# Kernel optimization log

Hardware: AMD Instinct MI355X
Metric: run time of the kernel (lower is better)

## Reference

```python
import jax, jax.numpy as jnp
import numpy as np


def setup_inputs() -> dict:
    key = jax.random.key(0)
    k1, k2 = jax.random.split(key)
    B, N, E, D = 8, 2048, 64, 128
    spatial_embedding = jax.random.normal(k1, (B, N, E), dtype=jnp.float32)
    z = jax.random.normal(k2, (B, N, D), dtype=jnp.float32)
    return {"spatial_embedding": spatial_embedding, "z": z}


def reference(spatial_embedding, z):
    # Pairwise squared L2 distance via ||a||^2 + ||b||^2 - 2 a.b
    # (same math as (e0-e1).norm(2,-1)**2, avoids [B,N,N,E] intermediate)
    sq = jnp.sum(spatial_embedding * spatial_embedding, axis=-1)  # [B,N]
    inner = jnp.einsum('bie,bje->bij', spatial_embedding, spatial_embedding)
    d2 = jnp.maximum(sq[:, :, None] + sq[:, None, :] - 2.0 * inner, 0.0)  # [B,N,N]
    sim = jnp.exp(-d2)
    attn = sim / jnp.sum(sim, axis=-1, keepdims=True)
    out = jnp.einsum('bij,bjd->bid', attn, z)
    return out
```

## Files before the change

### kernel.cpp

```cpp
#include <hip/hip_runtime.h>
#include <hip/hip_bf16.h>

#define BB 8
#define NN 2048
#define EE 64
#define DD 128
#define BN (BB * NN)

typedef __attribute__((ext_vector_type(8))) short short8v;
typedef __attribute__((ext_vector_type(4))) float float4v;

__device__ __forceinline__ short f2bf(float f) {
    __hip_bfloat16 h = __float2bfloat16(f);
    return *reinterpret_cast<short*>(&h);
}
__device__ __forceinline__ uint32_t pack2bf(float a, float b) {
    return (uint32_t)(uint16_t)f2bf(a) | ((uint32_t)(uint16_t)f2bf(b) << 16);
}

__global__ __launch_bounds__(256) void prep_kernel(const float* __restrict__ emb,
                                                   const float* __restrict__ z,
                                                   short* __restrict__ embq,
                                                   short* __restrict__ zq,
                                                   float* __restrict__ sq) {
    __shared__ float zl[64 * 129];
    const int bid = blockIdx.x;
    const int t = threadIdx.x;

    if (bid < 512) {
        int gid = bid * 256 + t;
        int s = gid & 63;
        int ke = (gid >> 6) & 1;
        int r16 = (gid >> 7) & 127;
        int b = gid >> 14;
        int i = r16 * 16 + (s & 15);
        int e0 = ke * 32 + ((s >> 4) & 3) * 8;
        const float4* src = reinterpret_cast<const float4*>(emb + ((size_t)(b * NN + i)) * EE + e0);
        float4 v0 = src[0], v1 = src[1];
        short8v o;
        o[0] = f2bf(v0.x); o[1] = f2bf(v0.y); o[2] = f2bf(v0.z); o[3] = f2bf(v0.w);
        o[4] = f2bf(v1.x); o[5] = f2bf(v1.y); o[6] = f2bf(v1.z); o[7] = f2bf(v1.w);
        *reinterpret_cast<short8v*>(embq + (size_t)gid * 8) = o;
    } else if (bid < 768) {
        int v = bid - 512;
        int b = v >> 5;
        int jt = v & 31;
        int jb = jt * 64;
#pragma unroll
        for (int k = 0; k < 8; ++k) {
            int idx = t + k * 256;
            int jl = idx >> 5, c4 = idx & 31;
            float4 w = reinterpret_cast<const float4*>(z + ((size_t)(b * NN + jb + jl)) * DD)[c4];
            float* p = &zl[jl * 129 + c4 * 4];
            p[0] = w.x; p[1] = w.y; p[2] = w.z; p[3] = w.w;
        }
        __syncthreads();
#pragma unroll
        for (int k = 0; k < 4; ++k) {
            int sid = t + k * 256;
            int blk = sid >> 6, s = sid & 63;
            int ktl = blk >> 3, nt = blk & 7;
            int d = nt * 16 + (s & 15);
            int jl = ktl * 32 + ((s >> 4) & 3) * 8;
            short8v o;
#pragma unroll
            for (int e = 0; e < 8; ++e) o[e] = f2bf(zl[(jl + e) * 129 + d]);
            *reinterpret_cast<short8v*>(zq + ((size_t)((b * 64 + jt * 2 + ktl) * 8 + nt) * 64 + s) * 8) = o;
        }
    } else {
        int v = bid - 768;
        int q = t & 15;
#pragma unroll
        for (int p = 0; p < 4; ++p) {
            int row = v * 64 + p * 16 + (t >> 4);
            float4 rv = reinterpret_cast<const float4*>(emb + (size_t)row * EE)[q];
            float a0 = __bfloat162float(__float2bfloat16(rv.x));
            float a1 = __bfloat162float(__float2bfloat16(rv.y));
            float a2 = __bfloat162float(__float2bfloat16(rv.z));
            float a3 = __bfloat162float(__float2bfloat16(rv.w));
            float s2 = a0 * a0 + a1 * a1 + a2 * a2 + a3 * a3;
#pragma unroll
            for (int off = 1; off < 16; off <<= 1) s2 += __shfl_xor(s2, off);
            if (q == 0) sq[row] = s2;
        }
    }
}

__global__ __launch_bounds__(256, 2) void attn_mfma(const short* __restrict__ embq,
                                                    const short* __restrict__ zq,
                                                    const float* __restrict__ sq,
                                                    float* __restrict__ outnum,
                                                    float* __restrict__ den,
                                                    int njs) {
    __shared__ short sU[4][2048];

    const int t = threadIdx.x;
    const int bid = blockIdx.x;
    const int b = bid & 7;
    const int q = bid >> 3;
    const int it = q & 15;
    const int js = q >> 4;
    const int ib = it * 128;
    const int w = t >> 6;
    const int l = t & 63;
    const int g = (l >> 4) & 3;
    const int c = l & 15;

    const short8v* embq8 = (const short8v*)embq;
    const short8v* zq8 = (const short8v*)zq;
    const float* sqB = sq + b * NN;

    const int ntiles = 32 / njs;
    const int jt0 = js * ntiles;
    const int jtEnd = jt0 + ntiles;

    short8v qkB[2][2];
#pragma unroll
    for (int m = 0; m < 2; ++m)
#pragma unroll
        for (int ke = 0; ke < 2; ++ke)
            qkB[m][ke] = embq8[((size_t)(b * 128 + it * 8 + w * 2 + m) * 2 + ke) * 64 + l];
    float sqi[2];
#pragma unroll
    for (int m = 0; m < 2; ++m) sqi[m] = sqB[ib + w * 32 + m * 16 + c];

    float dsum[2] = {0.f, 0.f};
    float4v acc[2][8];
#pragma unroll
    for (int m = 0; m < 2; ++m)
#pragma unroll
        for (int nt = 0; nt < 8; ++nt) acc[m][nt] = (float4v){0.f, 0.f, 0.f, 0.f};

    char* ptw = (char*)&sU[w][0];
    const int swz = (c & 7) << 4;

    for (int jt = jt0; jt < jtEnd; ++jt) {
        short8v a[4][2];
        float4 sqj[4];
#pragma unroll
        for (int J = 0; J < 4; ++J) {
            a[J][0] = embq8[((size_t)(b * 128 + jt * 4 + J) * 2 + 0) * 64 + l];
            a[J][1] = embq8[((size_t)(b * 128 + jt * 4 + J) * 2 + 1) * 64 + l];
            sqj[J] = *reinterpret_cast<const float4*>(sqB + jt * 64 + J * 16 + 4 * g);
        }

        bool anyLive = false;
#pragma unroll
        for (int J = 0; J < 4; ++J) {
            float d2[2][4];
            float mn = 1e30f;
#pragma unroll
            for (int m = 0; m < 2; ++m) {
                float4v sfr = (float4v){0.f, 0.f, 0.f, 0.f};
                sfr = __builtin_amdgcn_mfma_f32_16x16x32_bf16(a[J][0], qkB[m][0], sfr, 0, 0, 0);
                sfr = __builtin_amdgcn_mfma_f32_16x16x32_bf16(a[J][1], qkB[m][1], sfr, 0, 0, 0);
                d2[m][0] = fmaxf(fmaf(-2.0f, sfr[0], sqi[m] + sqj[J].x), 0.0f);
                d2[m][1] = fmaxf(fmaf(-2.0f, sfr[1], sqi[m] + sqj[J].y), 0.0f);
                d2[m][2] = fmaxf(fmaf(-2.0f, sfr[2], sqi[m] + sqj[J].z), 0.0f);
                d2[m][3] = fmaxf(fmaf(-2.0f, sfr[3], sqi[m] + sqj[J].w), 0.0f);
                mn = fminf(mn, fminf(fminf(d2[m][0], d2[m][1]), fminf(d2[m][2], d2[m][3])));
            }
            const bool live = !__all(mn > 13.8f);
#pragma unroll
            for (int m = 0; m < 2; ++m) {
                unsigned long long pword = 0ull;
                if (live) {
                    float p0 = __expf(-d2[m][0]);
                    float p1 = __expf(-d2[m][1]);
                    float p2 = __expf(-d2[m][2]);
                    float p3 = __expf(-d2[m][3]);
                    dsum[m] += (p0 + p1) + (p2 + p3);
                    pword = (unsigned long long)pack2bf(p0, p1) |
                            ((unsigned long long)pack2bf(p2, p3) << 32);
                }
                *reinterpret_cast<unsigned long long*>(
                    ptw + ((m * 2048 + c * 128 + g * 8) ^ swz ^ (J * 32))) = pword;
            }
            anyLive |= live;
        }

        if (anyLive) {
            short8v pa[2][2];
#pragma unroll
            for (int m = 0; m < 2; ++m)
#pragma unroll
                for (int kt = 0; kt < 2; ++kt)
                    pa[m][kt] = *reinterpret_cast<const short8v*>(
                        ptw + ((m * 2048 + c * 128 + kt * 64 + g * 16) ^ swz));
#pragma unroll
            for (int nt = 0; nt < 8; ++nt) {
                short8v z0 = zq8[(size_t)((b * 64 + jt * 2 + 0) * 8 + nt) * 64 + l];
                short8v z1 = zq8[(size_t)((b * 64 + jt * 2 + 1) * 8 + nt) * 64 + l];
#pragma unroll
                for (int m = 0; m < 2; ++m) {
                    acc[m][nt] = __builtin_amdgcn_mfma_f32_16x16x32_bf16(pa[m][0], z0, acc[m][nt], 0, 0, 0);
                    acc[m][nt] = __builtin_amdgcn_mfma_f32_16x16x32_bf16(pa[m][1], z1, acc[m][nt], 0, 0, 0);
                }
            }
        }
    }

#pragma unroll
    for (int m = 0; m < 2; ++m) {
        dsum[m] += __shfl_xor(dsum[m], 16);
        dsum[m] += __shfl_xor(dsum[m], 32);
    }

    if (njs == 1) {
#pragma unroll
        for (int m = 0; m < 2; ++m) {
            float invr[4];
#pragma unroll
            for (int r = 0; r < 4; ++r) invr[r] = 1.0f / __shfl(dsum[m], 4 * g + r);
#pragma unroll
            for (int r = 0; r < 4; ++r) {
                size_t row = (size_t)(b * NN + ib + w * 32 + m * 16 + 4 * g + r);
#pragma unroll
                for (int nt = 0; nt < 8; ++nt)
                    outnum[row * DD + nt * 16 + c] = acc[m][nt][r] * invr[r];
            }
        }
    } else {
        if (l < 16) {
            den[(size_t)js * BN + b * NN + ib + w * 32 + l] = dsum[0];
            den[(size_t)js * BN + b * NN + ib + w * 32 + 16 + l] = dsum[1];
        }
        if (!__all(fmaxf(dsum[0], dsum[1]) < 1e-6f)) {
#pragma unroll
            for (int m = 0; m < 2; ++m)
#pragma unroll
                for (int r = 0; r < 4; ++r) {
                    size_t row = (size_t)js * BN + b * NN + ib + w * 32 + m * 16 + 4 * g + r;
#pragma unroll
                    for (int nt = 0; nt < 8; ++nt)
                        outnum[row * DD + nt * 16 + c] = acc[m][nt][r];
                }
        }
    }
}

__global__ __launch_bounds__(256) void reduce_kernel(const float4* __restrict__ num,
                                                     const float* __restrict__ den,
                                                     float4* __restrict__ out,
                                                     int njs) {
    int i4 = blockIdx.x * 256 + threadIdx.x;
    int row = i4 >> 5;
    float4 ns = make_float4(0.f, 0.f, 0.f, 0.f);
    float ds = 0.f;
    for (int js = 0; js < njs; ++js) {
        float dj = den[(size_t)js * BN + row];
        ds += dj;
        if (dj >= 1e-6f) {
            float4 v = num[(size_t)js * ((size_t)BN * (DD / 4)) + i4];
            ns.x += v.x; ns.y += v.y; ns.z += v.z; ns.w += v.w;
        }
    }
    float inv = 1.0f / ds;
    out[i4] = make_float4(ns.x * inv, ns.y * inv, ns.z * inv, ns.w * inv);
}

extern "C" void kernel_launch(void* const* d_in, const int* in_sizes, int n_in,
                              void* d_out, int out_size, void* d_ws, size_t ws_size,
                              hipStream_t stream) {
    (void)in_sizes; (void)n_in; (void)out_size;
    const float* emb = (const float*)d_in[0];
    const float* z = (const float*)d_in[1];
    float* out = (float*)d_out;
    float* ws = (float*)d_ws;

    int njs = 1;
    if (ws_size >= 40ull * 1024 * 1024) njs = 4;
    else if (ws_size >= 24ull * 1024 * 1024) njs = 2;

    float* sqw = ws;
    float* denw = ws + BN;
    float* numw = denw + (size_t)njs * BN;
    size_t numFloats = (njs > 1) ? (size_t)njs * BN * DD : 0;
    short* embqw = (short*)(numw + numFloats);
    short* zqw = embqw + (size_t)BB * NN * EE;

    prep_kernel<<<1024, 256, 0, stream>>>(emb, z, embqw, zqw, sqw);

    attn_mfma<<<8 * 16 * njs, 256, 0, stream>>>(embqw, zqw, sqw,
                                                njs == 1 ? out : numw, denw, njs);

    if (njs > 1) {
        reduce_kernel<<<(BN * (DD / 4)) / 256, 256, 0, stream>>>(
            (const float4*)numw, denw, (float4*)out, njs);
    }
}
```

Baseline: 30.48 us.

## Split key range across wave pairs and reduce partial accumulators in LDS

Each block now covers 64 query rows instead of 128, and the grid doubles. Pairs of waves share a 32-row query slice and each processes half of the key tiles. Their partial numerators and denominators are then combined through shared memory with several barriers. Launch bounds are raised to 4 blocks per CU to hide latency better. The cost is extra LDS traffic, syncs and register pressure from the higher occupancy target, and the key-side loads are duplicated across more blocks.

```diff
diff --git a/kernel.cpp b/kernel.cpp
--- a/kernel.cpp
+++ b/kernel.cpp
@@ -86,22 +86,25 @@
     }
 }
 
-__global__ __launch_bounds__(256, 2) void attn_mfma(const short* __restrict__ embq,
+__global__ __launch_bounds__(256, 4) void attn_mfma(const short* __restrict__ embq,
                                                     const short* __restrict__ zq,
                                                     const float* __restrict__ sq,
                                                     float* __restrict__ outnum,
                                                     float* __restrict__ den,
                                                     int njs) {
     __shared__ short sU[4][2048];
+    __shared__ float sDn[2][2][64];
 
     const int t = threadIdx.x;
     const int bid = blockIdx.x;
     const int b = bid & 7;
     const int q = bid >> 3;
-    const int it = q & 15;
-    const int js = q >> 4;
-    const int ib = it * 128;
+    const int it = q & 31;
+    const int js = q >> 5;
+    const int ib = it * 64;
     const int w = t >> 6;
+    const int h = w >> 1;
+    const int u = w & 1;
     const int l = t & 63;
     const int g = (l >> 4) & 3;
     const int c = l & 15;
@@ -110,19 +113,19 @@
     const short8v* zq8 = (const short8v*)zq;
     const float* sqB = sq + b * NN;
 
-    const int ntiles = 32 / njs;
-    const int jt0 = js * ntiles;
-    const int jtEnd = jt0 + ntiles;
+    const int ntW = (32 / njs) >> 1;
+    const int jtW0 = js * (32 / njs) + u * ntW;
+    const int jtEnd = jtW0 + ntW;
 
     short8v qkB[2][2];
 #pragma unroll
     for (int m = 0; m < 2; ++m)
 #pragma unroll
         for (int ke = 0; ke < 2; ++ke)
-            qkB[m][ke] = embq8[((size_t)(b * 128 + it * 8 + w * 2 + m) * 2 + ke) * 64 + l];
+            qkB[m][ke] = embq8[((size_t)(b * 128 + it * 4 + h * 2 + m) * 2 + ke) * 64 + l];
     float sqi[2];
 #pragma unroll
-    for (int m = 0; m < 2; ++m) sqi[m] = sqB[ib + w * 32 + m * 16 + c];
+    for (int m = 0; m < 2; ++m) sqi[m] = sqB[ib + h * 32 + m * 16 + c];
 
     float dsum[2] = {0.f, 0.f};
     float4v acc[2][8];
@@ -134,7 +137,7 @@
     char* ptw = (char*)&sU[w][0];
     const int swz = (c & 7) << 4;
 
-    for (int jt = jt0; jt < jtEnd; ++jt) {
+    for (int jt = jtW0; jt < jtEnd; ++jt) {
         short8v a[4][2];
         float4 sqj[4];
 #pragma unroll
@@ -206,6 +209,31 @@
         dsum[m] += __shfl_xor(dsum[m], 32);
     }
 
+    float4v* sF = reinterpret_cast<float4v*>(&sU[0][0]);
+    __syncthreads();
+    if (u == 1) {
+#pragma unroll
+        for (int m = 0; m < 2; ++m) sDn[h][m][l] = dsum[m];
+#pragma unroll
+        for (int nt = 0; nt < 8; ++nt) sF[h * 512 + nt * 64 + l] = acc[0][nt];
+    }
+    __syncthreads();
+    if (u == 0) {
+#pragma unroll
+        for (int m = 0; m < 2; ++m) dsum[m] += sDn[h][m][l];
+#pragma unroll
+        for (int nt = 0; nt < 8; ++nt) acc[0][nt] += sF[h * 512 + nt * 64 + l];
+    }
+    __syncthreads();
+    if (u == 1) {
+#pragma unroll
+        for (int nt = 0; nt < 8; ++nt) sF[h * 512 + nt * 64 + l] = acc[1][nt];
+    }
+    __syncthreads();
+    if (u == 1) return;
+#pragma unroll
+    for (int nt = 0; nt < 8; ++nt) acc[1][nt] += sF[h * 512 + nt * 64 + l];
+
     if (njs == 1) {
 #pragma unroll
         for (int m = 0; m < 2; ++m) {
@@ -214,7 +242,7 @@
             for (int r = 0; r < 4; ++r) invr[r] = 1.0f / __shfl(dsum[m], 4 * g + r);
 #pragma unroll
             for (int r = 0; r < 4; ++r) {
-                size_t row = (size_t)(b * NN + ib + w * 32 + m * 16 + 4 * g + r);
+                size_t row = (size_t)(b * NN + ib + h * 32 + m * 16 + 4 * g + r);
 #pragma unroll
                 for (int nt = 0; nt < 8; ++nt)
                     outnum[row * DD + nt * 16 + c] = acc[m][nt][r] * invr[r];
@@ -222,15 +250,15 @@
         }
     } else {
         if (l < 16) {
-            den[(size_t)js * BN + b * NN + ib + w * 32 + l] = dsum[0];
-            den[(size_t)js * BN + b * NN + ib + w * 32 + 16 + l] = dsum[1];
+            den[(size_t)js * BN + b * NN + ib + h * 32 + l] = dsum[0];
+            den[(size_t)js * BN + b * NN + ib + h * 32 + 16 + l] = dsum[1];
         }
         if (!__all(fmaxf(dsum[0], dsum[1]) < 1e-6f)) {
 #pragma unroll
             for (int m = 0; m < 2; ++m)
 #pragma unroll
                 for (int r = 0; r < 4; ++r) {
-                    size_t row = (size_t)js * BN + b * NN + ib + w * 32 + m * 16 + 4 * g + r;
+                    size_t row = (size_t)js * BN + b * NN + ib + h * 32 + m * 16 + 4 * g + r;
 #pragma unroll
                     for (int nt = 0; nt < 8; ++nt)
                         outnum[row * DD + nt * 16 + c] = acc[m][nt][r];
@@ -281,7 +309,7 @@
 
     prep_kernel<<<1024, 256, 0, stream>>>(emb, z, embqw, zqw, sqw);
 
-    attn_mfma<<<8 * 16 * njs, 256, 0, stream>>>(embqw, zqw, sqw,
+    attn_mfma<<<8 * 32 * njs, 256, 0, stream>>>(embqw, zqw, sqw,
                                                 njs == 1 ? out : numw, denw, njs);
 
     if (njs > 1) {
```

Result: slower. 43.68 us (+43.3%).

## Double-buffer embedding tile loads and use a cheap lower bound for liveness

Applied to the files above, without the earlier changes.

Restructures the j-tile loop into a two-stage software pipeline: each embedding tile's fragments are loaded into registers one tile ahead, so the global load latency overlaps the MFMA and exp work of the current tile. It also replaces the per-element clamped distance computation used for the skip test with a cheaper lower bound built from the max inner product and the min column norm. Full distances are now computed only for live sub-tiles. The bound is more conservative, so fewer sub-tiles may be skipped. The prefetch reads one tile past the end of each work range, which for the last batch goes beyond the buffer, and the loop assumes an even tile count. The double buffer also adds register pressure.

```diff
diff --git a/kernel.cpp b/kernel.cpp
--- a/kernel.cpp
+++ b/kernel.cpp
@@ -86,6 +86,20 @@
     }
 }
 
+#define LOADA(dst, basep)                                                      \
+    do {                                                                       \
+        const char* _b0 = (basep);                                             \
+        const char* _b1 = (basep) + 4096;                                      \
+        dst[0][0] = *reinterpret_cast<const short8v*>(_b0);                    \
+        dst[0][1] = *reinterpret_cast<const short8v*>(_b0 + 1024);             \
+        dst[1][0] = *reinterpret_cast<const short8v*>(_b0 + 2048);             \
+        dst[1][1] = *reinterpret_cast<const short8v*>(_b0 + 3072);             \
+        dst[2][0] = *reinterpret_cast<const short8v*>(_b1);                    \
+        dst[2][1] = *reinterpret_cast<const short8v*>(_b1 + 1024);             \
+        dst[3][0] = *reinterpret_cast<const short8v*>(_b1 + 2048);             \
+        dst[3][1] = *reinterpret_cast<const short8v*>(_b1 + 3072);             \
+    } while (0)
+
 __global__ __launch_bounds__(256, 2) void attn_mfma(const short* __restrict__ embq,
                                                     const short* __restrict__ zq,
                                                     const float* __restrict__ sq,
@@ -110,9 +124,8 @@
     const short8v* zq8 = (const short8v*)zq;
     const float* sqB = sq + b * NN;
 
-    const int ntiles = 32 / njs;
-    const int jt0 = js * ntiles;
-    const int jtEnd = jt0 + ntiles;
+    const int ntW = 32 / njs;
+    const int jt0 = js * ntW;
 
     short8v qkB[2][2];
 #pragma unroll
@@ -134,41 +147,38 @@
     char* ptw = (char*)&sU[w][0];
     const int swz = (c & 7) << 4;
 
-    for (int jt = jt0; jt < jtEnd; ++jt) {
-        short8v a[4][2];
-        float4 sqj[4];
+    auto computeTile = [&](int jt, short8v (&A)[4][2]) {
+        const float* sqjp = sqB + jt * 64 + 4 * g;
+        bool anyLive = false;
+        float sfr[2][4];
+        float4 sqj;
 #pragma unroll
         for (int J = 0; J < 4; ++J) {
-            a[J][0] = embq8[((size_t)(b * 128 + jt * 4 + J) * 2 + 0) * 64 + l];
-            a[J][1] = embq8[((size_t)(b * 128 + jt * 4 + J) * 2 + 1) * 64 + l];
-            sqj[J] = *reinterpret_cast<const float4*>(sqB + jt * 64 + J * 16 + 4 * g);
-        }
-
-        bool anyLive = false;
-#pragma unroll
-        for (int J = 0; J < 4; ++J) {
-            float d2[2][4];
-            float mn = 1e30f;
+            sqj = *reinterpret_cast<const float4*>(sqjp + J * 16);
+            float sqjmin = fminf(fminf(sqj.x, sqj.y), fminf(sqj.z, sqj.w));
+            float bnd = 1e30f;
 #pragma unroll
             for (int m = 0; m < 2; ++m) {
-                float4v sfr = (float4v){0.f, 0.f, 0.f, 0.f};
-                sfr = __builtin_amdgcn_mfma_f32_16x16x32_bf16(a[J][0], qkB[m][0], sfr, 0, 0, 0);
-                sfr = __builtin_amdgcn_mfma_f32_16x16x32_bf16(a[J][1], qkB[m][1], sfr, 0, 0, 0);
-                d2[m][0] = fmaxf(fmaf(-2.0f, sfr[0], sqi[m] + sqj[J].x), 0.0f);
-                d2[m][1] = fmaxf(fmaf(-2.0f, sfr[1], sqi[m] + sqj[J].y), 0.0f);
-                d2[m][2] = fmaxf(fmaf(-2.0f, sfr[2], sqi[m] + sqj[J].z), 0.0f);
-                d2[m][3] = fmaxf(fmaf(-2.0f, sfr[3], sqi[m] + sqj[J].w), 0.0f);
-                mn = fminf(mn, fminf(fminf(d2[m][0], d2[m][1]), fminf(d2[m][2], d2[m][3])));
+                float4v sf = (float4v){0.f, 0.f, 0.f, 0.f};
+                sf = __builtin_amdgcn_mfma_f32_16x16x32_bf16(A[J][0], qkB[m][0], sf, 0, 0, 0);
+                sf = __builtin_amdgcn_mfma_f32_16x16x32_bf16(A[J][1], qkB[m][1], sf, 0, 0, 0);
+                sfr[m][0] = sf[0]; sfr[m][1] = sf[1]; sfr[m][2] = sf[2]; sfr[m][3] = sf[3];
+                float smax = fmaxf(fmaxf(sf[0], sf[1]), fmaxf(sf[2], sf[3]));
+                bnd = fminf(bnd, fmaf(-2.0f, smax, sqi[m] + sqjmin));
             }
-            const bool live = !__all(mn > 13.8f);
+            const bool liveJ = !__all(bnd > 13.8f);
 #pragma unroll
             for (int m = 0; m < 2; ++m) {
                 unsigned long long pword = 0ull;
-                if (live) {
-                    float p0 = __expf(-d2[m][0]);
-                    float p1 = __expf(-d2[m][1]);
-                    float p2 = __expf(-d2[m][2]);
-                    float p3 = __expf(-d2[m][3]);
+                if (liveJ) {
+                    float d0 = fmaxf(fmaf(-2.0f, sfr[m][0], sqi[m] + sqj.x), 0.0f);
+                    float d1 = fmaxf(fmaf(-2.0f, sfr[m][1], sqi[m] + sqj.y), 0.0f);
+                    float d2_ = fmaxf(fmaf(-2.0f, sfr[m][2], sqi[m] + sqj.z), 0.0f);
+                    float d3 = fmaxf(fmaf(-2.0f, sfr[m][3], sqi[m] + sqj.w), 0.0f);
+                    float p0 = __expf(-d0);
+                    float p1 = __expf(-d1);
+                    float p2 = __expf(-d2_);
+                    float p3 = __expf(-d3);
                     dsum[m] += (p0 + p1) + (p2 + p3);
                     pword = (unsigned long long)pack2bf(p0, p1) |
                             ((unsigned long long)pack2bf(p2, p3) << 32);
@@ -176,7 +186,7 @@
                 *reinterpret_cast<unsigned long long*>(
                     ptw + ((m * 2048 + c * 128 + g * 8) ^ swz ^ (J * 32))) = pword;
             }
-            anyLive |= live;
+            anyLive |= liveJ;
         }
 
         if (anyLive) {
@@ -198,6 +208,21 @@
                 }
             }
         }
+    };
+
+    const char* pa = (const char*)embq8 + (((size_t)(b * 128 + jt0 * 4) * 2) * 64 + l) * 16;
+
+    short8v A0[4][2], A1[4][2];
+    LOADA(A0, pa);
+
+    for (int jp = 0; jp < ntW / 2; ++jp) {
+        const int jt = jt0 + 2 * jp;
+        pa += 8192;
+        LOADA(A1, pa);
+        computeTile(jt, A0);
+        pa += 8192;
+        LOADA(A0, pa);
+        computeTile(jt + 1, A1);
     }
 
 #pragma unroll
```

New measurement: 31.02 us. Within noise of the previous version (+1.8%).
